# Kernel tuning notes

Measured on AMD Instinct MI355X. Metric: run time of the kernel, lower is better.

## Reference

```python
import jax, jax.numpy as jnp
import numpy as np

UNITS = 512

def gru_cell(x, h, W, U, b):
    # Keras GRUCell, reset_after=True (v2 / cuDNN-compatible formulation)
    # x: [B, D], h: [B, U], W: [D, 3U], U: [U, 3U], b: [2, 3U]
    bi, br = b[0], b[1]
    xg = x @ W + bi          # input gates  [B, 3U]
    hg = h @ U + br          # recurrent gates [B, 3U]
    xz, xr, xh = jnp.split(xg, 3, axis=-1)
    hz, hr, hh = jnp.split(hg, 3, axis=-1)
    z = jax.nn.sigmoid(xz + hz)
    r = jax.nn.sigmoid(xr + hr)
    cand = jnp.tanh(xh + r * hh)
    return z * h + (1.0 - z) * cand

def setup_inputs() -> dict:
    key = jax.random.key(0)
    ks = jax.random.split(key, 7)
    B, T, D, U = 64, 1024, 512, UNITS
    s_in = 1.0 / np.sqrt(D)
    s_rec = 1.0 / np.sqrt(U)
    return {
        "x":  jax.random.normal(ks[0], (B, T, D), dtype=jnp.float32),
        "W0": jax.random.normal(ks[1], (D, 3 * U), dtype=jnp.float32) * s_in,
        "U0": jax.random.normal(ks[2], (U, 3 * U), dtype=jnp.float32) * s_rec,
        "b0": jax.random.normal(ks[3], (2, 3 * U), dtype=jnp.float32) * 0.01,
        "W1": jax.random.normal(ks[4], (U, 3 * U), dtype=jnp.float32) * s_rec,
        "U1": jax.random.normal(ks[5], (U, 3 * U), dtype=jnp.float32) * s_rec,
        "b1": jax.random.normal(ks[6], (2, 3 * U), dtype=jnp.float32) * 0.01,
    }

def reference(x, W0, U0, b0, W1, U1, b1):
    B = x.shape[0]
    h0_init = jnp.zeros((B, UNITS), dtype=x.dtype)
    h1_init = jnp.zeros((B, UNITS), dtype=x.dtype)

    def step(carry, x_t):
        h0, h1 = carry
        h0 = gru_cell(x_t, h0, W0, U0, b0)   # cell 0 consumes input
        h1 = gru_cell(h0, h1, W1, U1, b1)    # cell 1 consumes cell 0 output
        return (h0, h1), None

    xs = jnp.swapaxes(x, 0, 1)  # [T, B, D] for scan over time
    (h0, h1), _ = jax.lax.scan(step, (h0_init, h1_init), xs)
    # RNN(return_sequences=False) returns last-step output of last cell
    return h1
```

## Files before the change

kernel.cpp:

```cpp
#include <hip/hip_runtime.h>


typedef __bf16 bf16x8 __attribute__((ext_vector_type(8)));
typedef float  f32x4  __attribute__((ext_vector_type(4)));
typedef unsigned int uint4v __attribute__((ext_vector_type(4)));

#define T_STEPS 1024
#define NWG 256
#define NTHR 256
#define SMEM_BYTES (98304 + 4096 + 1024 + 128 + 32)

__device__ __align__(16) unsigned int g_h0[1025LL * 64 * 512];
__device__ __align__(16) unsigned int g_h1[1025LL * 64 * 512];
__device__ unsigned int g_leaf[8 * 64];
__device__ unsigned int g_root[64];
__device__ unsigned int g_epoch[64];
__device__ __align__(256) unsigned int g_cnt[2][2][64];
__device__ __align__(256) unsigned int g_cntx[2][64];

__device__ __forceinline__ void f2hilo(float f, unsigned short& hi, unsigned short& lo) {
    __bf16 h = (__bf16)f;
    float  fh = (float)h;
    __bf16 l = (__bf16)(f - fh);
    hi = __builtin_bit_cast(unsigned short, h);
    lo = __builtin_bit_cast(unsigned short, l);
}

__device__ __forceinline__ f32x4 mfma16(bf16x8 a, bf16x8 b, f32x4 c) {
    return __builtin_amdgcn_mfma_f32_16x16x32_bf16(a, b, c, 0, 0, 0);
}

__device__ __forceinline__ void unpack8(const unsigned int* p, bf16x8& ah, bf16x8& al) {
    uint4v v0 = *(const uint4v*)p;
    uint4v v1 = *(const uint4v*)(p + 4);
    uint4v h, l;
    h.x = __builtin_amdgcn_perm(v0.y, v0.x, 0x07060302u);
    h.y = __builtin_amdgcn_perm(v0.w, v0.z, 0x07060302u);
    h.z = __builtin_amdgcn_perm(v1.y, v1.x, 0x07060302u);
    h.w = __builtin_amdgcn_perm(v1.w, v1.z, 0x07060302u);
    l.x = __builtin_amdgcn_perm(v0.y, v0.x, 0x05040100u);
    l.y = __builtin_amdgcn_perm(v0.w, v0.z, 0x05040100u);
    l.z = __builtin_amdgcn_perm(v1.y, v1.x, 0x05040100u);
    l.w = __builtin_amdgcn_perm(v1.w, v1.z, 0x05040100u);
    ah = __builtin_bit_cast(bf16x8, h);
    al = __builtin_bit_cast(bf16x8, l);
}

__device__ __forceinline__ void cvt8(const float* p, bf16x8& ah, bf16x8& al) {
    float4 a = *(const float4*)p;
    float4 b = *(const float4*)(p + 4);
    float f[8] = {a.x, a.y, a.z, a.w, b.x, b.y, b.z, b.w};
    bf16x8 h, l;
    #pragma unroll
    for (int i = 0; i < 8; ++i) {
        __bf16 hv = (__bf16)f[i];
        h[i] = hv;
        l[i] = (__bf16)(f[i] - (float)hv);
    }
    ah = h; al = l;
}

__device__ __forceinline__ void gemm_pass(
    bool useX, int pass, int ntile, int lane, int lcol, int kch,
    const float* A0x, const unsigned int* Ap,
    const unsigned short* sBhi, const unsigned short* sBlo,
    f32x4& acc_zr, f32x4& acc_xh, f32x4& acc_hh)
{
    bf16x8 bzero = {};
    if (ntile == 0) {
        #pragma unroll 4
        for (int ks = 0; ks < 16; ++ks) {
            bf16x8 ah, al;
            if (useX) cvt8(A0x + ks * 32 + kch * 8, ah, al);
            else      unpack8(Ap + ks * 32 + kch * 8, ah, al);
            const int o = pass * 12288 + ks * 512 + lane * 8;
            bf16x8 bh = *(const bf16x8*)(sBhi + o);
            bf16x8 bl = *(const bf16x8*)(sBlo + o);
            acc_zr = mfma16(ah, bh, acc_zr);
            acc_zr = mfma16(ah, bl, acc_zr);
            acc_zr = mfma16(al, bh, acc_zr);
        }
    } else {
        #pragma unroll 4
        for (int ks = 0; ks < 16; ++ks) {
            bf16x8 ah, al;
            if (useX) cvt8(A0x + ks * 32 + kch * 8, ah, al);
            else      unpack8(Ap + ks * 32 + kch * 8, ah, al);
            bf16x8 bh = bzero, bl = bzero;
            if (lcol < 8) {
                const int e = kch * 8 + lcol;
                const int o = pass * 12288 + 8192 + ks * 256 + e * 8;
                bh = *(const bf16x8*)(sBhi + o);
                bl = *(const bf16x8*)(sBlo + o);
            }
            f32x4 acc = pass ? acc_hh : acc_xh;
            acc = mfma16(ah, bh, acc);
            acc = mfma16(ah, bl, acc);
            acc = mfma16(al, bh, acc);
            if (pass) acc_hh = acc; else acc_xh = acc;
        }
    }
}

__device__ __forceinline__ float epilogue_hn(
    int tid, int mtile, int ntile, int lane, int lcol,
    const f32x4& acc_zr, const f32x4& acc_xh, const f32x4& acc_hh,
    float* sAcc, float* sHprev, const float* sBias)
{
    const int drow = mtile * 16 + (lane >> 4) * 4;
    if (ntile == 0) {
        #pragma unroll
        for (int r2 = 0; r2 < 4; ++r2) sAcc[(drow + r2) * 16 + lcol] = acc_zr[r2];
    } else if (lcol < 8) {
        #pragma unroll
        for (int r2 = 0; r2 < 4; ++r2) {
            sAcc[512 + (drow + r2) * 8 + lcol] = acc_xh[r2];
            sAcc[768 + (drow + r2) * 8 + lcol] = acc_hh[r2];
        }
    }
    __syncthreads();
    const int ml  = tid >> 3;
    const int col = tid & 7;
    const float zp = sAcc[ml * 16 + col]     + sBias[col];
    const float rp = sAcc[ml * 16 + 8 + col] + sBias[8 + col];
    const float z = 1.f / (1.f + __expf(-zp));
    const float r = 1.f / (1.f + __expf(-rp));
    const float xh = sAcc[512 + ml * 8 + col] + sBias[16 + col];
    const float hh = sAcc[768 + ml * 8 + col] + sBias[24 + col];
    const float ct = tanhf(xh + r * hh);
    const float hp = sHprev[tid];
    const float hn = z * hp + (1.f - z) * ct;
    sHprev[tid] = hn;
    return hn;
}

__device__ __forceinline__ void wait_cnt(unsigned int* C, unsigned int target, int tid) {
    if (tid == 0) {
        int spins = 0;
        while ((int)(__hip_atomic_load(C, __ATOMIC_RELAXED,
                                       __HIP_MEMORY_SCOPE_AGENT) - target) < 0) {
            if (spins < 4) __builtin_amdgcn_s_sleep(1);
            else           __builtin_amdgcn_s_sleep(8);
            ++spins;
        }
    }
    __syncthreads();
}

__global__ void __launch_bounds__(NTHR, 1) gru_persistent(
    const float* __restrict__ x,  const float* __restrict__ W0,
    const float* __restrict__ U0, const float* __restrict__ b0,
    const float* __restrict__ W1, const float* __restrict__ U1,
    const float* __restrict__ b1, float* __restrict__ out)
{
    extern __shared__ char smem[];
    unsigned short* sBhi = (unsigned short*)smem;
    unsigned short* sBlo = sBhi + 24576;
    float* sAcc   = (float*)(smem + 98304);
    float* sHprev = sAcc + 1024;
    float* sBias  = sHprev + 256;
    unsigned int* sE0 = (unsigned int*)(sBias + 32);

    const int wg    = blockIdx.x;
    const int g     = wg >> 7;
    const int cell  = (wg >> 6) & 1;
    const int slice = wg & 63;
    const int c0    = slice * 8;
    const int tid   = threadIdx.x;

    __builtin_amdgcn_fence(__ATOMIC_ACQUIRE, "agent");

    if (tid == 0) {
        sE0[0] = __hip_atomic_load(&g_epoch[0], __ATOMIC_RELAXED, __HIP_MEMORY_SCOPE_AGENT);
        sE0[1] = __hip_atomic_load(&g_cnt[cell][g][0], __ATOMIC_RELAXED, __HIP_MEMORY_SCOPE_AGENT);
        sE0[2] = __hip_atomic_load(&g_cntx[g][0], __ATOMIC_RELAXED, __HIP_MEMORY_SCOPE_AGENT);
    }

    {
        const int ml = tid >> 3, col = tid & 7;
        unsigned int* dst = (cell ? g_h1 : g_h0)
                          + (long long)(g * 32 + ml) * 512 + (c0 + col);
        __hip_atomic_store(dst, 0u, __ATOMIC_RELAXED, __HIP_MEMORY_SCOPE_AGENT);
    }

    {
        const float* Wm = cell ? W1 : W0;
        const float* Um = cell ? U1 : U0;
        for (int e = tid; e < 24576; e += NTHR) {
            const int pass = e / 12288;
            const int rem  = e % 12288;
            int j, gcol;
            if (rem < 8192) {
                const int ks = rem >> 9, r2 = rem & 511;
                const int entry = r2 >> 3, i = r2 & 7;
                const int col = entry & 15, kch = entry >> 4;
                j = ks * 32 + kch * 8 + i;
                gcol = (col < 8) ? (c0 + col) : (512 + c0 + col - 8);
            } else {
                const int r2 = rem - 8192;
                const int ks = r2 >> 8, r3 = r2 & 255;
                const int entry = r3 >> 3, i = r3 & 7;
                const int col = entry & 7, kch = entry >> 3;
                j = ks * 32 + kch * 8 + i;
                gcol = 1024 + c0 + col;
            }
            const float v = (pass ? Um : Wm)[j * 1536 + gcol];
            f2hilo(v, sBhi[e], sBlo[e]);
        }
    }
    {
        const float* b = cell ? b1 : b0;
        if (tid < 32) {
            const int col = tid & 7, sec = tid >> 3;
            float v;
            if (sec == 0)      v = b[c0 + col] + b[1536 + c0 + col];
            else if (sec == 1) v = b[512 + c0 + col] + b[1536 + 512 + c0 + col];
            else if (sec == 2) v = b[1024 + c0 + col];
            else               v = b[1536 + 1024 + c0 + col];
            sBias[tid] = v;
        }
        sHprev[tid] = 0.f;
    }
    __syncthreads();
    const unsigned int E0     = sE0[0];
    const unsigned int Cown   = sE0[1];
    const unsigned int Ccross = sE0[2];

    {
        const unsigned int target = E0 + 1u;
        if (tid == 0) {
            asm volatile("s_waitcnt vmcnt(0)" ::: "memory");
            unsigned int o = __hip_atomic_fetch_add(&g_leaf[(wg & 7) * 64], 1u,
                                __ATOMIC_RELAXED, __HIP_MEMORY_SCOPE_AGENT);
            if (o == 32u * target - 1u) {
                unsigned int r = __hip_atomic_fetch_add(&g_root[0], 1u,
                                    __ATOMIC_RELAXED, __HIP_MEMORY_SCOPE_AGENT);
                if (r == 8u * target - 1u)
                    __hip_atomic_store(&g_epoch[0], target,
                                       __ATOMIC_RELAXED, __HIP_MEMORY_SCOPE_AGENT);
            }
        }
        while ((int)(__hip_atomic_load(&g_epoch[0], __ATOMIC_RELAXED,
                                       __HIP_MEMORY_SCOPE_AGENT) - target) < 0)
            __builtin_amdgcn_s_sleep(1);
        asm volatile("" ::: "memory");
        __syncthreads();
    }

    const int lane  = tid & 63;
    const int mtile = (tid >> 6) & 1;
    const int ntile = tid >> 7;
    const int lcol  = lane & 15;
    const int kch   = lane >> 4;
    const int arow  = g * 32 + mtile * 16 + lcol;
    const int ml    = tid >> 3;
    const int colw  = tid & 7;

    if (cell == 0) {
        unsigned int* const cnt  = &g_cnt[0][g][0];
        unsigned int* const cntx = &g_cntx[g][0];
        for (int k = 0; k < T_STEPS; ++k) {
            f32x4 acc_zr = {0.f, 0.f, 0.f, 0.f};
            f32x4 acc_xh = {0.f, 0.f, 0.f, 0.f};
            f32x4 acc_hh = {0.f, 0.f, 0.f, 0.f};
            const float* A0x = x + ((long long)arow * 1024 + k) * 512;
            gemm_pass(true, 0, ntile, lane, lcol, kch, A0x, nullptr,
                      sBhi, sBlo, acc_zr, acc_xh, acc_hh);

            if (k > 0) wait_cnt(cnt, Cown + 64u * (unsigned int)k, tid);

            const unsigned int* A1p = g_h0 + ((long long)k * (64 * 512)) + arow * 512;
            gemm_pass(false, 1, ntile, lane, lcol, kch, nullptr, A1p,
                      sBhi, sBlo, acc_zr, acc_xh, acc_hh);

            const float hn = epilogue_hn(tid, mtile, ntile, lane, lcol,
                                         acc_zr, acc_xh, acc_hh, sAcc, sHprev, sBias);
            {
                unsigned short hi_, lo_;
                f2hilo(hn, hi_, lo_);
                const unsigned int pk = ((unsigned int)hi_ << 16) | (unsigned int)lo_;
                unsigned int* dst = g_h0 + (long long)(k + 1) * (64 * 512)
                                  + (long long)(g * 32 + ml) * 512 + (c0 + colw);
                __hip_atomic_store(dst, pk, __ATOMIC_RELAXED, __HIP_MEMORY_SCOPE_AGENT);
            }
            __syncthreads();
            if (tid == 0) {
                __hip_atomic_fetch_add(cnt, 1u, __ATOMIC_RELAXED, __HIP_MEMORY_SCOPE_AGENT);
                __hip_atomic_fetch_add(cntx, 1u, __ATOMIC_RELAXED, __HIP_MEMORY_SCOPE_AGENT);
            }
        }
    } else {
        unsigned int* const cnt   = &g_cnt[1][g][0];
        unsigned int* const cntUp = &g_cntx[g][0];
        for (int t = 0; t < T_STEPS; ++t) {
            if (t > 0) wait_cnt(cnt, Cown + 64u * (unsigned int)t, tid);

            f32x4 acc_zr = {0.f, 0.f, 0.f, 0.f};
            f32x4 acc_xh = {0.f, 0.f, 0.f, 0.f};
            f32x4 acc_hh = {0.f, 0.f, 0.f, 0.f};

            const unsigned int* A1p = g_h1 + ((long long)t * (64 * 512)) + arow * 512;
            gemm_pass(false, 1, ntile, lane, lcol, kch, nullptr, A1p,
                      sBhi, sBlo, acc_zr, acc_xh, acc_hh);

            wait_cnt(cntUp, Ccross + 64u * (unsigned int)(t + 1), tid);

            const unsigned int* A0p = g_h0 + ((long long)(t + 1) * (64 * 512)) + arow * 512;
            gemm_pass(false, 0, ntile, lane, lcol, kch, nullptr, A0p,
                      sBhi, sBlo, acc_zr, acc_xh, acc_hh);

            const float hn = epilogue_hn(tid, mtile, ntile, lane, lcol,
                                         acc_zr, acc_xh, acc_hh, sAcc, sHprev, sBias);
            {
                unsigned short hi_, lo_;
                f2hilo(hn, hi_, lo_);
                const unsigned int pk = ((unsigned int)hi_ << 16) | (unsigned int)lo_;
                unsigned int* dst = g_h1 + (long long)(t + 1) * (64 * 512)
                                  + (long long)(g * 32 + ml) * 512 + (c0 + colw);
                __hip_atomic_store(dst, pk, __ATOMIC_RELAXED, __HIP_MEMORY_SCOPE_AGENT);
                if (t == T_STEPS - 1)
                    out[(g * 32 + ml) * 512 + (c0 + colw)] = hn;
            }
            __syncthreads();
            if (tid == 0)
                __hip_atomic_fetch_add(cnt, 1u, __ATOMIC_RELAXED, __HIP_MEMORY_SCOPE_AGENT);
        }
    }
}

extern "C" void kernel_launch(void* const* d_in, const int* in_sizes, int n_in,
                              void* d_out, int out_size, void* d_ws, size_t ws_size,
                              hipStream_t stream) {
    (void)in_sizes; (void)n_in; (void)d_ws; (void)ws_size; (void)out_size;
    const float* x  = (const float*)d_in[0];
    const float* W0 = (const float*)d_in[1];
    const float* U0 = (const float*)d_in[2];
    const float* b0 = (const float*)d_in[3];
    const float* W1 = (const float*)d_in[4];
    const float* U1 = (const float*)d_in[5];
    const float* b1 = (const float*)d_in[6];
    float* out = (float*)d_out;

    (void)hipFuncSetAttribute((const void*)gru_persistent,
                              hipFuncAttributeMaxDynamicSharedMemorySize, SMEM_BYTES);
    void* args[] = {&x, &W0, &U0, &b0, &W1, &U1, &b1, &out};
    hipError_t e = hipLaunchCooperativeKernel((const void*)gru_persistent,
                                              dim3(NWG), dim3(NTHR),
                                              args, SMEM_BYTES, stream);
    if (e != hipSuccess) {
        gru_persistent<<<dim3(NWG), dim3(NTHR), SMEM_BYTES, stream>>>(
            x, W0, U0, b0, W1, U1, b1, out);
    }
}
```

Before: 9.986 ms.

## Precompute input projection for cell 0 across all WGs and switch to per-slice flags

Before the recurrence, all 256 workgroups compute x@W0 for every timestep into a global buffer, so cell 0's per-step loop skips the input GEMM pass and only reads precomputed gate values. Counter-based atomic barriers are replaced by per-slice epoch flags polled by 64 threads with a wave-wide all-reduce, avoiding contended fetch_add. Loop unroll is raised to 8 and hprev is kept in a register. This adds a large global buffer and a prologue GEMM, and cell 1 must repack its weights afterwards.

Result: slower. 15.86 ms (+58.8%).

```diff
diff --git a/kernel.cpp b/kernel.cpp
--- a/kernel.cpp
+++ b/kernel.cpp
@@ -12,11 +12,11 @@
 
 __device__ __align__(16) unsigned int g_h0[1025LL * 64 * 512];
 __device__ __align__(16) unsigned int g_h1[1025LL * 64 * 512];
+__device__ __align__(16) float g_xg[1024LL * 64 * 2 * 32 * 24];
 __device__ unsigned int g_leaf[8 * 64];
 __device__ unsigned int g_root[64];
 __device__ unsigned int g_epoch[64];
-__device__ __align__(256) unsigned int g_cnt[2][2][64];
-__device__ __align__(256) unsigned int g_cntx[2][64];
+__device__ __align__(256) unsigned int g_flags[2][2][256];
 
 __device__ __forceinline__ void f2hilo(float f, unsigned short& hi, unsigned short& lo) {
     __bf16 h = (__bf16)f;
@@ -68,7 +68,7 @@
 {
     bf16x8 bzero = {};
     if (ntile == 0) {
-        #pragma unroll 4
+        #pragma unroll 8
         for (int ks = 0; ks < 16; ++ks) {
             bf16x8 ah, al;
             if (useX) cvt8(A0x + ks * 32 + kch * 8, ah, al);
@@ -81,7 +81,7 @@
             acc_zr = mfma16(al, bh, acc_zr);
         }
     } else {
-        #pragma unroll 4
+        #pragma unroll 8
         for (int ks = 0; ks < 16; ++ks) {
             bf16x8 ah, al;
             if (useX) cvt8(A0x + ks * 32 + kch * 8, ah, al);
@@ -102,10 +102,38 @@
     }
 }
 
+__device__ __forceinline__ void pack_weights(
+    const float* Wm, const float* Um, int c0, int tid,
+    unsigned short* sBhi, unsigned short* sBlo)
+{
+    for (int e = tid; e < 24576; e += NTHR) {
+        const int pass = e / 12288;
+        const int rem  = e % 12288;
+        int j, gcol;
+        if (rem < 8192) {
+            const int ks = rem >> 9, r2 = rem & 511;
+            const int entry = r2 >> 3, i = r2 & 7;
+            const int col = entry & 15, kch = entry >> 4;
+            j = ks * 32 + kch * 8 + i;
+            gcol = (col < 8) ? (c0 + col) : (512 + c0 + col - 8);
+        } else {
+            const int r2 = rem - 8192;
+            const int ks = r2 >> 8, r3 = r2 & 255;
+            const int entry = r3 >> 3, i = r3 & 7;
+            const int col = entry & 7, kch = entry >> 3;
+            j = ks * 32 + kch * 8 + i;
+            gcol = 1024 + c0 + col;
+        }
+        const float v = (pass ? Um : Wm)[j * 1536 + gcol];
+        f2hilo(v, sBhi[e], sBlo[e]);
+    }
+}
+
 __device__ __forceinline__ float epilogue_hn(
     int tid, int mtile, int ntile, int lane, int lcol,
     const f32x4& acc_zr, const f32x4& acc_xh, const f32x4& acc_hh,
-    float* sAcc, float* sHprev, const float* sBias)
+    float* sAcc, const float* sBias, float hp,
+    bool useXg, float xgz, float xgr, float xgh)
 {
     const int drow = mtile * 16 + (lane >> 4) * 4;
     if (ntile == 0) {
@@ -114,34 +142,31 @@
     } else if (lcol < 8) {
         #pragma unroll
         for (int r2 = 0; r2 < 4; ++r2) {
-            sAcc[512 + (drow + r2) * 8 + lcol] = acc_xh[r2];
+            if (!useXg) sAcc[512 + (drow + r2) * 8 + lcol] = acc_xh[r2];
             sAcc[768 + (drow + r2) * 8 + lcol] = acc_hh[r2];
         }
     }
     __syncthreads();
     const int ml  = tid >> 3;
     const int col = tid & 7;
-    const float zp = sAcc[ml * 16 + col]     + sBias[col];
-    const float rp = sAcc[ml * 16 + 8 + col] + sBias[8 + col];
+    float zp = sAcc[ml * 16 + col]     + sBias[col];
+    float rp = sAcc[ml * 16 + 8 + col] + sBias[8 + col];
+    if (useXg) { zp += xgz; rp += xgr; }
     const float z = 1.f / (1.f + __expf(-zp));
     const float r = 1.f / (1.f + __expf(-rp));
-    const float xh = sAcc[512 + ml * 8 + col] + sBias[16 + col];
+    const float xh = (useXg ? xgh : sAcc[512 + ml * 8 + col]) + sBias[16 + col];
     const float hh = sAcc[768 + ml * 8 + col] + sBias[24 + col];
     const float ct = tanhf(xh + r * hh);
-    const float hp = sHprev[tid];
-    const float hn = z * hp + (1.f - z) * ct;
-    sHprev[tid] = hn;
-    return hn;
-}
-
-__device__ __forceinline__ void wait_cnt(unsigned int* C, unsigned int target, int tid) {
-    if (tid == 0) {
-        int spins = 0;
-        while ((int)(__hip_atomic_load(C, __ATOMIC_RELAXED,
-                                       __HIP_MEMORY_SCOPE_AGENT) - target) < 0) {
-            if (spins < 4) __builtin_amdgcn_s_sleep(1);
-            else           __builtin_amdgcn_s_sleep(8);
-            ++spins;
+    return z * hp + (1.f - z) * ct;
+}
+
+__device__ __forceinline__ void wait_flags(unsigned int* F, unsigned int target, int tid) {
+    if (tid < 64) {
+        for (;;) {
+            unsigned int v = __hip_atomic_load(&F[tid * 4], __ATOMIC_RELAXED,
+                                               __HIP_MEMORY_SCOPE_AGENT);
+            if (__all((int)(v - target) >= 0)) break;
+            __builtin_amdgcn_s_sleep(1);
         }
     }
     __syncthreads();
@@ -157,8 +182,7 @@
     unsigned short* sBhi = (unsigned short*)smem;
     unsigned short* sBlo = sBhi + 24576;
     float* sAcc   = (float*)(smem + 98304);
-    float* sHprev = sAcc + 1024;
-    float* sBias  = sHprev + 256;
+    float* sBias  = sAcc + 1024 + 256;
     unsigned int* sE0 = (unsigned int*)(sBias + 32);
 
     const int wg    = blockIdx.x;
@@ -170,44 +194,18 @@
 
     __builtin_amdgcn_fence(__ATOMIC_ACQUIRE, "agent");
 
-    if (tid == 0) {
+    if (tid == 0)
         sE0[0] = __hip_atomic_load(&g_epoch[0], __ATOMIC_RELAXED, __HIP_MEMORY_SCOPE_AGENT);
-        sE0[1] = __hip_atomic_load(&g_cnt[cell][g][0], __ATOMIC_RELAXED, __HIP_MEMORY_SCOPE_AGENT);
-        sE0[2] = __hip_atomic_load(&g_cntx[g][0], __ATOMIC_RELAXED, __HIP_MEMORY_SCOPE_AGENT);
-    }
 
     {
-        const int ml = tid >> 3, col = tid & 7;
+        const int mlz = tid >> 3, colz = tid & 7;
         unsigned int* dst = (cell ? g_h1 : g_h0)
-                          + (long long)(g * 32 + ml) * 512 + (c0 + col);
+                          + (long long)(g * 32 + mlz) * 512 + (c0 + colz);
         __hip_atomic_store(dst, 0u, __ATOMIC_RELAXED, __HIP_MEMORY_SCOPE_AGENT);
     }
 
-    {
-        const float* Wm = cell ? W1 : W0;
-        const float* Um = cell ? U1 : U0;
-        for (int e = tid; e < 24576; e += NTHR) {
-            const int pass = e / 12288;
-            const int rem  = e % 12288;
-            int j, gcol;
-            if (rem < 8192) {
-                const int ks = rem >> 9, r2 = rem & 511;
-                const int entry = r2 >> 3, i = r2 & 7;
-                const int col = entry & 15, kch = entry >> 4;
-                j = ks * 32 + kch * 8 + i;
-                gcol = (col < 8) ? (c0 + col) : (512 + c0 + col - 8);
-            } else {
-                const int r2 = rem - 8192;
-                const int ks = r2 >> 8, r3 = r2 & 255;
-                const int entry = r3 >> 3, i = r3 & 7;
-                const int col = entry & 7, kch = entry >> 3;
-                j = ks * 32 + kch * 8 + i;
-                gcol = 1024 + c0 + col;
-            }
-            const float v = (pass ? Um : Wm)[j * 1536 + gcol];
-            f2hilo(v, sBhi[e], sBlo[e]);
-        }
-    }
+    pack_weights(W0, U0, c0, tid, sBhi, sBlo);
+
     {
         const float* b = cell ? b1 : b0;
         if (tid < 32) {
@@ -219,12 +217,56 @@
             else               v = b[1536 + 1024 + c0 + col];
             sBias[tid] = v;
         }
-        sHprev[tid] = 0.f;
     }
     __syncthreads();
-    const unsigned int E0     = sE0[0];
-    const unsigned int Cown   = sE0[1];
-    const unsigned int Ccross = sE0[2];
+    const unsigned int E0 = sE0[0];
+    const unsigned int EB = (E0 + 1u) << 10;
+
+    const int lane  = tid & 63;
+    const int mtile = (tid >> 6) & 1;
+    const int ntile = tid >> 7;
+    const int lcol  = lane & 15;
+    const int kch   = lane >> 4;
+    const int arow  = g * 32 + mtile * 16 + lcol;
+    const int ml    = tid >> 3;
+    const int colw  = tid & 7;
+
+    {
+        const int q = wg >> 6;
+        for (int bb = 0; bb < 64; ++bb) {
+            for (int j = 0; j < 8; ++j) {
+                const int t0 = q * 256 + j * 32;
+                f32x4 acc_zr = {0.f, 0.f, 0.f, 0.f};
+                f32x4 acc_xh = {0.f, 0.f, 0.f, 0.f};
+                f32x4 acc_hh = {0.f, 0.f, 0.f, 0.f};
+                const float* A = x + ((long long)bb * 1024 + t0 + mtile * 16 + lcol) * 512;
+                gemm_pass(true, 0, ntile, lane, lcol, kch, A, nullptr,
+                          sBhi, sBlo, acc_zr, acc_xh, acc_hh);
+                __syncthreads();
+                const int drow = mtile * 16 + (lane >> 4) * 4;
+                if (ntile == 0) {
+                    #pragma unroll
+                    for (int r2 = 0; r2 < 4; ++r2) sAcc[(drow + r2) * 16 + lcol] = acc_zr[r2];
+                } else if (lcol < 8) {
+                    #pragma unroll
+                    for (int r2 = 0; r2 < 4; ++r2) sAcc[512 + (drow + r2) * 8 + lcol] = acc_xh[r2];
+                }
+                __syncthreads();
+                const float zv = sAcc[ml * 16 + colw];
+                const float rv = sAcc[ml * 16 + 8 + colw];
+                const float hv = sAcc[512 + ml * 8 + colw];
+                float* dst = g_xg + (long long)(t0 + ml) * 98304
+                           + slice * 1536 + (bb >> 5) * 768 + (bb & 31) * 24 + colw;
+                __hip_atomic_store((unsigned int*)dst,
+                    __builtin_bit_cast(unsigned int, zv), __ATOMIC_RELAXED, __HIP_MEMORY_SCOPE_AGENT);
+                __hip_atomic_store((unsigned int*)(dst + 8),
+                    __builtin_bit_cast(unsigned int, rv), __ATOMIC_RELAXED, __HIP_MEMORY_SCOPE_AGENT);
+                __hip_atomic_store((unsigned int*)(dst + 16),
+                    __builtin_bit_cast(unsigned int, hv), __ATOMIC_RELAXED, __HIP_MEMORY_SCOPE_AGENT);
+            }
+        }
+    }
+    __syncthreads();
 
     {
         const unsigned int target = E0 + 1u;
@@ -247,34 +289,34 @@
         __syncthreads();
     }
 
-    const int lane  = tid & 63;
-    const int mtile = (tid >> 6) & 1;
-    const int ntile = tid >> 7;
-    const int lcol  = lane & 15;
-    const int kch   = lane >> 4;
-    const int arow  = g * 32 + mtile * 16 + lcol;
-    const int ml    = tid >> 3;
-    const int colw  = tid & 7;
+    if (cell == 1) {
+        pack_weights(W1, U1, c0, tid, sBhi, sBlo);
+        __syncthreads();
+    }
+
+    float hprev = 0.f;
 
     if (cell == 0) {
-        unsigned int* const cnt  = &g_cnt[0][g][0];
-        unsigned int* const cntx = &g_cntx[g][0];
+        unsigned int* const myF  = &g_flags[0][g][slice * 4];
+        unsigned int* const ownF = &g_flags[0][g][0];
         for (int k = 0; k < T_STEPS; ++k) {
+            const float* xgp = g_xg + (long long)k * 98304
+                             + slice * 1536 + g * 768 + ml * 24 + colw;
+            const float xgz = xgp[0], xgr = xgp[8], xgh = xgp[16];
+
+            if (k > 0) wait_flags(ownF, EB + (unsigned int)k, tid);
+
             f32x4 acc_zr = {0.f, 0.f, 0.f, 0.f};
             f32x4 acc_xh = {0.f, 0.f, 0.f, 0.f};
             f32x4 acc_hh = {0.f, 0.f, 0.f, 0.f};
-            const float* A0x = x + ((long long)arow * 1024 + k) * 512;
-            gemm_pass(true, 0, ntile, lane, lcol, kch, A0x, nullptr,
-                      sBhi, sBlo, acc_zr, acc_xh, acc_hh);
-
-            if (k > 0) wait_cnt(cnt, Cown + 64u * (unsigned int)k, tid);
-
-            const unsigned int* A1p = g_h0 + ((long long)k * (64 * 512)) + arow * 512;
+            const unsigned int* A1p = g_h0 + (long long)k * (64 * 512) + arow * 512;
             gemm_pass(false, 1, ntile, lane, lcol, kch, nullptr, A1p,
                       sBhi, sBlo, acc_zr, acc_xh, acc_hh);
 
             const float hn = epilogue_hn(tid, mtile, ntile, lane, lcol,
-                                         acc_zr, acc_xh, acc_hh, sAcc, sHprev, sBias);
+                                         acc_zr, acc_xh, acc_hh, sAcc, sBias,
+                                         hprev, true, xgz, xgr, xgh);
+            hprev = hn;
             {
                 unsigned short hi_, lo_;
                 f2hilo(hn, hi_, lo_);
@@ -284,33 +326,35 @@
                 __hip_atomic_store(dst, pk, __ATOMIC_RELAXED, __HIP_MEMORY_SCOPE_AGENT);
             }
             __syncthreads();
-            if (tid == 0) {
-                __hip_atomic_fetch_add(cnt, 1u, __ATOMIC_RELAXED, __HIP_MEMORY_SCOPE_AGENT);
-                __hip_atomic_fetch_add(cntx, 1u, __ATOMIC_RELAXED, __HIP_MEMORY_SCOPE_AGENT);
-            }
+            if (tid == 0)
+                __hip_atomic_store(myF, EB + (unsigned int)(k + 1),
+                                   __ATOMIC_RELAXED, __HIP_MEMORY_SCOPE_AGENT);
         }
     } else {
-        unsigned int* const cnt   = &g_cnt[1][g][0];
-        unsigned int* const cntUp = &g_cntx[g][0];
+        unsigned int* const myF  = &g_flags[1][g][slice * 4];
+        unsigned int* const ownF = &g_flags[1][g][0];
+        unsigned int* const upF  = &g_flags[0][g][0];
         for (int t = 0; t < T_STEPS; ++t) {
-            if (t > 0) wait_cnt(cnt, Cown + 64u * (unsigned int)t, tid);
+            if (t > 0) wait_flags(ownF, EB + (unsigned int)t, tid);
 
             f32x4 acc_zr = {0.f, 0.f, 0.f, 0.f};
             f32x4 acc_xh = {0.f, 0.f, 0.f, 0.f};
             f32x4 acc_hh = {0.f, 0.f, 0.f, 0.f};
 
-            const unsigned int* A1p = g_h1 + ((long long)t * (64 * 512)) + arow * 512;
+            const unsigned int* A1p = g_h1 + (long long)t * (64 * 512) + arow * 512;
             gemm_pass(false, 1, ntile, lane, lcol, kch, nullptr, A1p,
                       sBhi, sBlo, acc_zr, acc_xh, acc_hh);
 
-            wait_cnt(cntUp, Ccross + 64u * (unsigned int)(t + 1), tid);
-
-            const unsigned int* A0p = g_h0 + ((long long)(t + 1) * (64 * 512)) + arow * 512;
+            wait_flags(upF, EB + (unsigned int)(t + 1), tid);
+
+            const unsigned int* A0p = g_h0 + (long long)(t + 1) * (64 * 512) + arow * 512;
             gemm_pass(false, 0, ntile, lane, lcol, kch, nullptr, A0p,
                       sBhi, sBlo, acc_zr, acc_xh, acc_hh);
 
             const float hn = epilogue_hn(tid, mtile, ntile, lane, lcol,
-                                         acc_zr, acc_xh, acc_hh, sAcc, sHprev, sBias);
+                                         acc_zr, acc_xh, acc_hh, sAcc, sBias,
+                                         hprev, false, 0.f, 0.f, 0.f);
+            hprev = hn;
             {
                 unsigned short hi_, lo_;
                 f2hilo(hn, hi_, lo_);
@@ -323,7 +367,8 @@
             }
             __syncthreads();
             if (tid == 0)
-                __hip_atomic_fetch_add(cnt, 1u, __ATOMIC_RELAXED, __HIP_MEMORY_SCOPE_AGENT);
+                __hip_atomic_store(myF, EB + (unsigned int)(t + 1),
+                                   __ATOMIC_RELAXED, __HIP_MEMORY_SCOPE_AGENT);
         }
     }
 }
```
